# Kernel optimization log

Measured on AMD Instinct MI355X. Metric: run time of the kernel, lower is better.

Reference implementation:

```python
import jax, jax.numpy as jnp
import numpy as np

N = 100000
E = 1600000
K = 3
D_IN = 128
D_OUT = 128


def setup_inputs() -> dict:
    key = jax.random.key(0)
    ks = jax.random.split(key, 12)
    x = jax.random.normal(ks[0], (N, D_IN), dtype=jnp.float32)
    edge_index = jax.random.randint(ks[1], (2, E), 0, N, dtype=jnp.int64)
    hop_src = jax.random.randint(ks[2], (K, E), 0, N, dtype=jnp.int64)
    hop_dst = jax.random.randint(ks[3], (K, E), 0, N, dtype=jnp.int64)
    hop_vals = jax.random.uniform(ks[4], (K, E), dtype=jnp.float32) / 16.0  # ~normalized adj
    s = 1.0 / np.sqrt(D_IN)
    W_short = jax.random.normal(ks[5], (D_IN, D_OUT), dtype=jnp.float32) * s
    att_short_w = jax.random.normal(ks[6], (2 * D_OUT, 1), dtype=jnp.float32) * 0.05
    att_short_b = jnp.zeros((1,), dtype=jnp.float32)
    W_long = jax.random.normal(ks[7], (D_IN, D_OUT), dtype=jnp.float32) * s
    att_long_w = jax.random.normal(ks[8], (D_OUT, 1), dtype=jnp.float32) * 0.05
    att_long_b = jnp.zeros((1,), dtype=jnp.float32)
    return {"x": x, "edge_index": edge_index, "hop_src": hop_src, "hop_dst": hop_dst,
            "hop_vals": hop_vals, "W_short": W_short, "att_short_w": att_short_w,
            "att_short_b": att_short_b, "W_long": W_long, "att_long_w": att_long_w,
            "att_long_b": att_long_b}


def _leaky(x, slope):
    return jnp.where(x >= 0, x, slope * x)


def reference(x, edge_index, hop_src, hop_dst, hop_vals, W_short, att_short_w,
              att_short_b, W_long, att_long_w, att_long_b):
    # ---- ShortDistanceAttention (GAT-style gather-compute-scatter) ----
    h = x @ W_short                                   # [N, D]
    # att([x_i, x_j]) = x_i @ w[:D] + x_j @ w[D:] + b  (precompute per-node scalars)
    a_i = (h @ att_short_w[:D_OUT]).squeeze(-1)       # [N]
    a_j = (h @ att_short_w[D_OUT:]).squeeze(-1)       # [N]
    src, dst = edge_index[0], edge_index[1]
    score = jnp.exp(_leaky(a_i[dst] + a_j[src] + att_short_b[0], 0.2))  # [E]
    short = jax.ops.segment_sum(score[:, None] * h[src], dst, num_segments=N)  # [N, D]

    # ---- LongDistanceAttention (per-hop spmm + hop-softmax fusion) ----
    def hop_emb(s_idx, d_idx, vals):
        agg = jax.ops.segment_sum(vals[:, None] * x[s_idx], d_idx, num_segments=N)  # A_k @ x
        return _leaky(agg @ W_long, 0.01)             # [N, D]

    hk = jax.vmap(hop_emb)(hop_src, hop_dst, hop_vals)   # [K, N, D]
    hk = jnp.transpose(hk, (1, 0, 2))                    # [N, K, D]
    logits = hk @ att_long_w + att_long_b                # [N, K, 1]
    attn = jax.nn.softmax(logits, axis=1)                # softmax over hops
    long = jnp.sum(attn * hk, axis=1)                    # [N, D]

    return short + long
```

## Files before the change

### kernel.cpp

```cpp
#include <hip/hip_runtime.h>
#include <hip/hip_bf16.h>

#define NN 100000
#define EE 1600000
#define KK 3
#define DD 128
#define CAP 48

static __device__ __forceinline__ unsigned short f2bf(float f) {
  __hip_bfloat16 b = __float2bfloat16(f);
  return *reinterpret_cast<unsigned short*>(&b);
}

__global__ __launch_bounds__(256) void gemm_hy_kernel(
    const float* __restrict__ x, const float* __restrict__ Ws,
    const float* __restrict__ Wl, unsigned short* __restrict__ hb,
    unsigned short* __restrict__ yb, int N) {
  __shared__ float xs[64][36];
  __shared__ float ws[32][128];
  __shared__ float wl[32][128];

  const int n0 = blockIdx.x * 64;
  const int t = threadIdx.x;
  const int tc = t & 31;
  const int tr = t >> 5;
  const int col = tc * 4;
  const int row = tr * 8;

  float acch[8][4], accy[8][4];
#pragma unroll
  for (int i = 0; i < 8; ++i)
#pragma unroll
    for (int j = 0; j < 4; ++j) { acch[i][j] = 0.f; accy[i][j] = 0.f; }

  for (int kc = 0; kc < DD; kc += 32) {
    {
      int r = t >> 3;
      int c4 = (t & 7) * 4;
      int gn0 = n0 + r;
      int gn1 = n0 + r + 32;
      float4 v0 = make_float4(0, 0, 0, 0), v1 = make_float4(0, 0, 0, 0);
      if (gn0 < N) v0 = *(const float4*)&x[(size_t)gn0 * DD + kc + c4];
      if (gn1 < N) v1 = *(const float4*)&x[(size_t)gn1 * DD + kc + c4];
      *(float4*)&xs[r][c4] = v0;
      *(float4*)&xs[r + 32][c4] = v1;
    }
    {
      int c4w = (t & 31) * 4;
      int kr0 = t >> 5;
#pragma unroll
      for (int i = 0; i < 4; ++i) {
        int kr = kr0 + i * 8;
        *(float4*)&ws[kr][c4w] = *(const float4*)&Ws[(size_t)(kc + kr) * DD + c4w];
        *(float4*)&wl[kr][c4w] = *(const float4*)&Wl[(size_t)(kc + kr) * DD + c4w];
      }
    }
    __syncthreads();
#pragma unroll 4
    for (int kk = 0; kk < 32; ++kk) {
      float a[8];
#pragma unroll
      for (int i = 0; i < 8; ++i) a[i] = xs[row + i][kk];
      float4 b = *(const float4*)&ws[kk][col];
      float4 c = *(const float4*)&wl[kk][col];
#pragma unroll
      for (int i = 0; i < 8; ++i) {
        acch[i][0] += a[i] * b.x; acch[i][1] += a[i] * b.y;
        acch[i][2] += a[i] * b.z; acch[i][3] += a[i] * b.w;
        accy[i][0] += a[i] * c.x; accy[i][1] += a[i] * c.y;
        accy[i][2] += a[i] * c.z; accy[i][3] += a[i] * c.w;
      }
    }
    __syncthreads();
  }
#pragma unroll
  for (int i = 0; i < 8; ++i) {
    int gn = n0 + row + i;
    if (gn < N) {
      ushort4 oh, oy;
      oh.x = f2bf(acch[i][0]); oh.y = f2bf(acch[i][1]);
      oh.z = f2bf(acch[i][2]); oh.w = f2bf(acch[i][3]);
      oy.x = f2bf(accy[i][0]); oy.y = f2bf(accy[i][1]);
      oy.z = f2bf(accy[i][2]); oy.w = f2bf(accy[i][3]);
      *(ushort4*)&hb[(size_t)gn * DD + col] = oh;
      *(ushort4*)&yb[(size_t)gn * DD + col] = oy;
    }
  }
}

__global__ __launch_bounds__(256) void a_kernel(
    const unsigned short* __restrict__ hb, const float* __restrict__ asw,
    float* __restrict__ a_i, float* __restrict__ a_j, int N) {
  int n = (blockIdx.x * 256 + threadIdx.x) >> 6;
  if (n >= N) return;
  int lane = threadIdx.x & 63;
  unsigned int u = ((const unsigned int*)hb)[(size_t)n * (DD / 2) + lane];
  float v0 = __uint_as_float(u << 16);
  float v1 = __uint_as_float(u & 0xffff0000u);
  float2 wi = *(const float2*)&asw[lane * 2];
  float2 wj = *(const float2*)&asw[DD + lane * 2];
  float si = v0 * wi.x + v1 * wi.y;
  float sj = v0 * wj.x + v1 * wj.y;
#pragma unroll
  for (int m = 32; m > 0; m >>= 1) {
    si += __shfl_down(si, m);
    sj += __shfl_down(sj, m);
  }
  if (lane == 0) {
    a_i[n] = si;
    a_j[n] = sj;
  }
}

__global__ __launch_bounds__(256) void fill_short_kernel(
    const int* __restrict__ ei, const float* __restrict__ a_i,
    const float* __restrict__ a_j, const float* __restrict__ bias,
    int* __restrict__ cnt, int2* __restrict__ pair, int E) {
  float b = bias[0];
  for (int e = blockIdx.x * 256 + threadIdx.x; e < E; e += gridDim.x * 256) {
    int src = ei[e];
    int dst = ei[E + e];
    float z = a_i[dst] + a_j[src] + b;
    float sc = expf(z >= 0.f ? z : 0.2f * z);
    int pos = atomicAdd(&cnt[dst], 1);
    if (pos < CAP) pair[(size_t)dst * CAP + pos] = make_int2(src, __float_as_int(sc));
  }
}

__global__ __launch_bounds__(256) void fill_hop_kernel(
    const int* __restrict__ hsrc, const int* __restrict__ hdst,
    const float* __restrict__ hvals, int* __restrict__ cnt,
    int2* __restrict__ pair, int E) {
  for (int e = blockIdx.x * 256 + threadIdx.x; e < E; e += gridDim.x * 256) {
    int src = hsrc[e];
    int dst = hdst[e];
    float v = hvals[e];
    int pos = atomicAdd(&cnt[dst], 1);
    if (pos < CAP) pair[(size_t)dst * CAP + pos] = make_int2(src, __float_as_int(v));
  }
}

__global__ __launch_bounds__(256) void fused_pull_kernel(
    const int* __restrict__ cnt, const int2* __restrict__ pairs,
    const unsigned short* __restrict__ hb, const unsigned short* __restrict__ yb,
    const float* __restrict__ alw, const float* __restrict__ alb,
    float* __restrict__ out, int N) {
  int n = (blockIdx.x * 256 + threadIdx.x) >> 6;
  if (n >= N) return;
  int lane = threadIdx.x & 63;
  const unsigned int* hp = (const unsigned int*)hb;
  const unsigned int* yp = (const unsigned int*)yb;

  float sx = 0.f, sy = 0.f;
  {
    const int2* pb = pairs + (size_t)n * CAP;
    int d = min(cnt[n], CAP);
    int j = 0;
    for (; j + 1 < d; j += 2) {
      int2 p0 = pb[j], p1 = pb[j + 1];
      unsigned int u0 = hp[(size_t)p0.x * (DD / 2) + lane];
      unsigned int u1 = hp[(size_t)p1.x * (DD / 2) + lane];
      float w0 = __int_as_float(p0.y), w1 = __int_as_float(p1.y);
      sx += w0 * __uint_as_float(u0 << 16);
      sy += w0 * __uint_as_float(u0 & 0xffff0000u);
      sx += w1 * __uint_as_float(u1 << 16);
      sy += w1 * __uint_as_float(u1 & 0xffff0000u);
    }
    if (j < d) {
      int2 p = pb[j];
      unsigned int u = hp[(size_t)p.x * (DD / 2) + lane];
      float w = __int_as_float(p.y);
      sx += w * __uint_as_float(u << 16);
      sy += w * __uint_as_float(u & 0xffff0000u);
    }
  }

  float gx[3], gy[3];
#pragma unroll
  for (int k = 0; k < 3; ++k) {
    const int2* pb = pairs + ((size_t)(k + 1) * NN + n) * CAP;
    int d = min(cnt[(k + 1) * NN + n], CAP);
    float ax = 0.f, ay = 0.f;
    int j = 0;
    for (; j + 1 < d; j += 2) {
      int2 p0 = pb[j], p1 = pb[j + 1];
      unsigned int u0 = yp[(size_t)p0.x * (DD / 2) + lane];
      unsigned int u1 = yp[(size_t)p1.x * (DD / 2) + lane];
      float w0 = __int_as_float(p0.y), w1 = __int_as_float(p1.y);
      ax += w0 * __uint_as_float(u0 << 16);
      ay += w0 * __uint_as_float(u0 & 0xffff0000u);
      ax += w1 * __uint_as_float(u1 << 16);
      ay += w1 * __uint_as_float(u1 & 0xffff0000u);
    }
    if (j < d) {
      int2 p = pb[j];
      unsigned int u = yp[(size_t)p.x * (DD / 2) + lane];
      float w = __int_as_float(p.y);
      ax += w * __uint_as_float(u << 16);
      ay += w * __uint_as_float(u & 0xffff0000u);
    }
    gx[k] = ax >= 0.f ? ax : 0.01f * ax;
    gy[k] = ay >= 0.f ? ay : 0.01f * ay;
  }

  float2 aw = *(const float2*)&alw[lane * 2];
  float bl = alb[0];
  float lg[3];
#pragma unroll
  for (int k = 0; k < 3; ++k) {
    float p = gx[k] * aw.x + gy[k] * aw.y;
#pragma unroll
    for (int m = 1; m < 64; m <<= 1) p += __shfl_xor(p, m);
    lg[k] = p + bl;
  }
  float mx = fmaxf(lg[0], fmaxf(lg[1], lg[2]));
  float e0 = expf(lg[0] - mx), e1 = expf(lg[1] - mx), e2 = expf(lg[2] - mx);
  float inv = 1.f / (e0 + e1 + e2);
  e0 *= inv; e1 *= inv; e2 *= inv;

  float ox = sx + e0 * gx[0] + e1 * gx[1] + e2 * gx[2];
  float oy = sy + e0 * gy[0] + e1 * gy[1] + e2 * gy[2];
  *(float2*)&out[(size_t)n * DD + lane * 2] = make_float2(ox, oy);
}

extern "C" void kernel_launch(void* const* d_in, const int* in_sizes, int n_in,
                              void* d_out, int out_size, void* d_ws, size_t ws_size,
                              hipStream_t stream) {
  const float* x        = (const float*)d_in[0];
  const int*   ei       = (const int*)d_in[1];
  const int*   hsrc     = (const int*)d_in[2];
  const int*   hdst     = (const int*)d_in[3];
  const float* hvals    = (const float*)d_in[4];
  const float* W_short  = (const float*)d_in[5];
  const float* asw      = (const float*)d_in[6];
  const float* asb      = (const float*)d_in[7];
  const float* W_long   = (const float*)d_in[8];
  const float* alw      = (const float*)d_in[9];
  const float* alb      = (const float*)d_in[10];
  float* out = (float*)d_out;

  unsigned short* hb = (unsigned short*)d_ws;
  unsigned short* yb = hb + (size_t)NN * DD;
  float* a_i = (float*)(yb + (size_t)NN * DD);
  float* a_j = a_i + NN;
  int*   cnt = (int*)(a_j + NN);
  int2*  pair = (int2*)(cnt + 4 * NN);

  const int FG = 4096;
  const int PG = (NN * 64 + 255) / 256;
  const int GG = (NN + 63) / 64;

  gemm_hy_kernel<<<GG, 256, 0, stream>>>(x, W_short, W_long, hb, yb, NN);
  a_kernel<<<PG, 256, 0, stream>>>(hb, asw, a_i, a_j, NN);

  hipMemsetAsync(cnt, 0, 4 * NN * sizeof(int), stream);
  fill_short_kernel<<<FG, 256, 0, stream>>>(ei, a_i, a_j, asb, cnt, pair, EE);
  for (int k = 0; k < KK; ++k)
    fill_hop_kernel<<<FG, 256, 0, stream>>>(hsrc + (size_t)k * EE,
                                            hdst + (size_t)k * EE,
                                            hvals + (size_t)k * EE,
                                            cnt + (size_t)(k + 1) * NN,
                                            pair + (size_t)(k + 1) * NN * CAP, EE);

  fused_pull_kernel<<<PG, 256, 0, stream>>>(cnt, pair, hb, yb, alw, alb, out, NN);
}
```

Baseline: 982.6 us.

## Merge fill kernels and interleave four neighbor lists in pull kernel

Replaces the four per-list fill launches with a single kernel over all edge lists. Restructures the pull kernel so each wave stages its four neighbor lists in LDS, splits into half-waves that process alternating edges with 8-byte bf16 loads, and interleaves the short and three hop gathers in one loop. The goal is to raise memory-level parallelism in the gather-bound pull and cut launch overhead. In exchange it adds LDS traffic, divergent branches and a cross-half reduction, and lowers the fill grid size.

```diff
diff --git a/kernel.cpp b/kernel.cpp
--- a/kernel.cpp
+++ b/kernel.cpp
@@ -10,6 +10,12 @@
 static __device__ __forceinline__ unsigned short f2bf(float f) {
   __hip_bfloat16 b = __float2bfloat16(f);
   return *reinterpret_cast<unsigned short*>(&b);
+}
+static __device__ __forceinline__ float bflo(unsigned int v) {
+  return __uint_as_float(v << 16);
+}
+static __device__ __forceinline__ float bfhi(unsigned int v) {
+  return __uint_as_float(v & 0xffff0000u);
 }
 
 __global__ __launch_bounds__(256) void gemm_hy_kernel(
@@ -95,8 +101,8 @@
   if (n >= N) return;
   int lane = threadIdx.x & 63;
   unsigned int u = ((const unsigned int*)hb)[(size_t)n * (DD / 2) + lane];
-  float v0 = __uint_as_float(u << 16);
-  float v1 = __uint_as_float(u & 0xffff0000u);
+  float v0 = bflo(u);
+  float v1 = bfhi(u);
   float2 wi = *(const float2*)&asw[lane * 2];
   float2 wj = *(const float2*)&asw[DD + lane * 2];
   float si = v0 * wi.x + v1 * wi.y;
@@ -112,31 +118,35 @@
   }
 }
 
-__global__ __launch_bounds__(256) void fill_short_kernel(
-    const int* __restrict__ ei, const float* __restrict__ a_i,
-    const float* __restrict__ a_j, const float* __restrict__ bias,
-    int* __restrict__ cnt, int2* __restrict__ pair, int E) {
+__global__ __launch_bounds__(256) void fill_all_kernel(
+    const int* __restrict__ ei, const int* __restrict__ hsrc,
+    const int* __restrict__ hdst, const float* __restrict__ hvals,
+    const float* __restrict__ a_i, const float* __restrict__ a_j,
+    const float* __restrict__ bias, int* __restrict__ cnt,
+    int2* __restrict__ pair) {
   float b = bias[0];
-  for (int e = blockIdx.x * 256 + threadIdx.x; e < E; e += gridDim.x * 256) {
-    int src = ei[e];
-    int dst = ei[E + e];
-    float z = a_i[dst] + a_j[src] + b;
-    float sc = expf(z >= 0.f ? z : 0.2f * z);
-    int pos = atomicAdd(&cnt[dst], 1);
-    if (pos < CAP) pair[(size_t)dst * CAP + pos] = make_int2(src, __float_as_int(sc));
-  }
-}
-
-__global__ __launch_bounds__(256) void fill_hop_kernel(
-    const int* __restrict__ hsrc, const int* __restrict__ hdst,
-    const float* __restrict__ hvals, int* __restrict__ cnt,
-    int2* __restrict__ pair, int E) {
-  for (int e = blockIdx.x * 256 + threadIdx.x; e < E; e += gridDim.x * 256) {
-    int src = hsrc[e];
-    int dst = hdst[e];
-    float v = hvals[e];
-    int pos = atomicAdd(&cnt[dst], 1);
-    if (pos < CAP) pair[(size_t)dst * CAP + pos] = make_int2(src, __float_as_int(v));
+  const long TOT = 4L * EE;
+  for (long s = (long)blockIdx.x * 256 + threadIdx.x; s < TOT;
+       s += (long)gridDim.x * 256) {
+    int list = (int)(s / EE);
+    int e = (int)(s - (long)list * EE);
+    int src, dst;
+    float wv;
+    if (list == 0) {
+      src = ei[e];
+      dst = ei[EE + e];
+      float z = a_i[dst] + a_j[src] + b;
+      wv = expf(z >= 0.f ? z : 0.2f * z);
+    } else {
+      int k = list - 1;
+      src = hsrc[(size_t)k * EE + e];
+      dst = hdst[(size_t)k * EE + e];
+      wv = hvals[(size_t)k * EE + e];
+    }
+    int pos = atomicAdd(&cnt[(size_t)list * NN + dst], 1);
+    if (pos < CAP)
+      pair[((size_t)list * NN + dst) * CAP + pos] =
+          make_int2(src, __float_as_int(wv));
   }
 }
 
@@ -145,82 +155,111 @@
     const unsigned short* __restrict__ hb, const unsigned short* __restrict__ yb,
     const float* __restrict__ alw, const float* __restrict__ alb,
     float* __restrict__ out, int N) {
+  __shared__ int2 plds[4][4][CAP];
   int n = (blockIdx.x * 256 + threadIdx.x) >> 6;
   if (n >= N) return;
-  int lane = threadIdx.x & 63;
-  const unsigned int* hp = (const unsigned int*)hb;
-  const unsigned int* yp = (const unsigned int*)yb;
-
-  float sx = 0.f, sy = 0.f;
-  {
-    const int2* pb = pairs + (size_t)n * CAP;
-    int d = min(cnt[n], CAP);
-    int j = 0;
-    for (; j + 1 < d; j += 2) {
-      int2 p0 = pb[j], p1 = pb[j + 1];
-      unsigned int u0 = hp[(size_t)p0.x * (DD / 2) + lane];
-      unsigned int u1 = hp[(size_t)p1.x * (DD / 2) + lane];
-      float w0 = __int_as_float(p0.y), w1 = __int_as_float(p1.y);
-      sx += w0 * __uint_as_float(u0 << 16);
-      sy += w0 * __uint_as_float(u0 & 0xffff0000u);
-      sx += w1 * __uint_as_float(u1 << 16);
-      sy += w1 * __uint_as_float(u1 & 0xffff0000u);
-    }
-    if (j < d) {
-      int2 p = pb[j];
-      unsigned int u = hp[(size_t)p.x * (DD / 2) + lane];
-      float w = __int_as_float(p.y);
-      sx += w * __uint_as_float(u << 16);
-      sy += w * __uint_as_float(u & 0xffff0000u);
-    }
-  }
-
-  float gx[3], gy[3];
-#pragma unroll
-  for (int k = 0; k < 3; ++k) {
-    const int2* pb = pairs + ((size_t)(k + 1) * NN + n) * CAP;
-    int d = min(cnt[(k + 1) * NN + n], CAP);
-    float ax = 0.f, ay = 0.f;
-    int j = 0;
-    for (; j + 1 < d; j += 2) {
-      int2 p0 = pb[j], p1 = pb[j + 1];
-      unsigned int u0 = yp[(size_t)p0.x * (DD / 2) + lane];
-      unsigned int u1 = yp[(size_t)p1.x * (DD / 2) + lane];
-      float w0 = __int_as_float(p0.y), w1 = __int_as_float(p1.y);
-      ax += w0 * __uint_as_float(u0 << 16);
-      ay += w0 * __uint_as_float(u0 & 0xffff0000u);
-      ax += w1 * __uint_as_float(u1 << 16);
-      ay += w1 * __uint_as_float(u1 & 0xffff0000u);
-    }
-    if (j < d) {
-      int2 p = pb[j];
-      unsigned int u = yp[(size_t)p.x * (DD / 2) + lane];
-      float w = __int_as_float(p.y);
-      ax += w * __uint_as_float(u << 16);
-      ay += w * __uint_as_float(u & 0xffff0000u);
-    }
-    gx[k] = ax >= 0.f ? ax : 0.01f * ax;
-    gy[k] = ay >= 0.f ? ay : 0.01f * ay;
-  }
-
-  float2 aw = *(const float2*)&alw[lane * 2];
+  const int wv = threadIdx.x >> 6;
+  const int lane = threadIdx.x & 63;
+  const int half = lane >> 5;
+  const int l32 = lane & 31;
+
+  const uint2* hp = (const uint2*)hb;
+  const uint2* yp = (const uint2*)yb;
+
+  const int d0 = min(cnt[n], CAP);
+  const int d1 = min(cnt[NN + n], CAP);
+  const int d2 = min(cnt[2 * NN + n], CAP);
+  const int d3 = min(cnt[3 * NN + n], CAP);
+
+  if (lane < d0) plds[wv][0][lane] = pairs[(size_t)n * CAP + lane];
+  if (lane < d1) plds[wv][1][lane] = pairs[((size_t)NN + n) * CAP + lane];
+  if (lane < d2) plds[wv][2][lane] = pairs[((size_t)2 * NN + n) * CAP + lane];
+  if (lane < d3) plds[wv][3][lane] = pairs[((size_t)3 * NN + n) * CAP + lane];
+
+  float s0[4] = {0, 0, 0, 0};
+  float g0[4] = {0, 0, 0, 0}, g1[4] = {0, 0, 0, 0}, g2[4] = {0, 0, 0, 0};
+
+  int maxd = max(max(d0, d1), max(d2, d3));
+  for (int j = half; j < maxd; j += 2) {
+    uint2 u0, u1, u2, u3;
+    float w0 = 0.f, w1 = 0.f, w2 = 0.f, w3 = 0.f;
+    if (j < d0) {
+      int2 p = plds[wv][0][j];
+      w0 = __int_as_float(p.y);
+      u0 = hp[(size_t)p.x * 32 + l32];
+    }
+    if (j < d1) {
+      int2 p = plds[wv][1][j];
+      w1 = __int_as_float(p.y);
+      u1 = yp[(size_t)p.x * 32 + l32];
+    }
+    if (j < d2) {
+      int2 p = plds[wv][2][j];
+      w2 = __int_as_float(p.y);
+      u2 = yp[(size_t)p.x * 32 + l32];
+    }
+    if (j < d3) {
+      int2 p = plds[wv][3][j];
+      w3 = __int_as_float(p.y);
+      u3 = yp[(size_t)p.x * 32 + l32];
+    }
+    if (j < d0) {
+      s0[0] += w0 * bflo(u0.x); s0[1] += w0 * bfhi(u0.x);
+      s0[2] += w0 * bflo(u0.y); s0[3] += w0 * bfhi(u0.y);
+    }
+    if (j < d1) {
+      g0[0] += w1 * bflo(u1.x); g0[1] += w1 * bfhi(u1.x);
+      g0[2] += w1 * bflo(u1.y); g0[3] += w1 * bfhi(u1.y);
+    }
+    if (j < d2) {
+      g1[0] += w2 * bflo(u2.x); g1[1] += w2 * bfhi(u2.x);
+      g1[2] += w2 * bflo(u2.y); g1[3] += w2 * bfhi(u2.y);
+    }
+    if (j < d3) {
+      g2[0] += w3 * bflo(u3.x); g2[1] += w3 * bfhi(u3.x);
+      g2[2] += w3 * bflo(u3.y); g2[3] += w3 * bfhi(u3.y);
+    }
+  }
+
+#pragma unroll
+  for (int c = 0; c < 4; ++c) {
+    s0[c] += __shfl_xor(s0[c], 32);
+    g0[c] += __shfl_xor(g0[c], 32);
+    g1[c] += __shfl_xor(g1[c], 32);
+    g2[c] += __shfl_xor(g2[c], 32);
+    g0[c] = g0[c] >= 0.f ? g0[c] : 0.01f * g0[c];
+    g1[c] = g1[c] >= 0.f ? g1[c] : 0.01f * g1[c];
+    g2[c] = g2[c] >= 0.f ? g2[c] : 0.01f * g2[c];
+  }
+
+  float4 aw = *(const float4*)&alw[l32 * 4];
   float bl = alb[0];
   float lg[3];
-#pragma unroll
-  for (int k = 0; k < 3; ++k) {
-    float p = gx[k] * aw.x + gy[k] * aw.y;
-#pragma unroll
-    for (int m = 1; m < 64; m <<= 1) p += __shfl_xor(p, m);
-    lg[k] = p + bl;
+  {
+    float p0 = g0[0] * aw.x + g0[1] * aw.y + g0[2] * aw.z + g0[3] * aw.w;
+    float p1 = g1[0] * aw.x + g1[1] * aw.y + g1[2] * aw.z + g1[3] * aw.w;
+    float p2 = g2[0] * aw.x + g2[1] * aw.y + g2[2] * aw.z + g2[3] * aw.w;
+#pragma unroll
+    for (int m = 1; m < 32; m <<= 1) {
+      p0 += __shfl_xor(p0, m);
+      p1 += __shfl_xor(p1, m);
+      p2 += __shfl_xor(p2, m);
+    }
+    lg[0] = p0 + bl; lg[1] = p1 + bl; lg[2] = p2 + bl;
   }
   float mx = fmaxf(lg[0], fmaxf(lg[1], lg[2]));
   float e0 = expf(lg[0] - mx), e1 = expf(lg[1] - mx), e2 = expf(lg[2] - mx);
   float inv = 1.f / (e0 + e1 + e2);
   e0 *= inv; e1 *= inv; e2 *= inv;
 
-  float ox = sx + e0 * gx[0] + e1 * gx[1] + e2 * gx[2];
-  float oy = sy + e0 * gy[0] + e1 * gy[1] + e2 * gy[2];
-  *(float2*)&out[(size_t)n * DD + lane * 2] = make_float2(ox, oy);
+  if (half == 0) {
+    float4 o;
+    o.x = s0[0] + e0 * g0[0] + e1 * g1[0] + e2 * g2[0];
+    o.y = s0[1] + e0 * g0[1] + e1 * g1[1] + e2 * g2[1];
+    o.z = s0[2] + e0 * g0[2] + e1 * g1[2] + e2 * g2[2];
+    o.w = s0[3] + e0 * g0[3] + e1 * g1[3] + e2 * g2[3];
+    *(float4*)&out[(size_t)n * DD + l32 * 4] = o;
+  }
 }
 
 extern "C" void kernel_launch(void* const* d_in, const int* in_sizes, int n_in,
@@ -246,7 +285,7 @@
   int*   cnt = (int*)(a_j + NN);
   int2*  pair = (int2*)(cnt + 4 * NN);
 
-  const int FG = 4096;
+  const int FG = 2048;
   const int PG = (NN * 64 + 255) / 256;
   const int GG = (NN + 63) / 64;
 
@@ -254,13 +293,8 @@
   a_kernel<<<PG, 256, 0, stream>>>(hb, asw, a_i, a_j, NN);
 
   hipMemsetAsync(cnt, 0, 4 * NN * sizeof(int), stream);
-  fill_short_kernel<<<FG, 256, 0, stream>>>(ei, a_i, a_j, asb, cnt, pair, EE);
-  for (int k = 0; k < KK; ++k)
-    fill_hop_kernel<<<FG, 256, 0, stream>>>(hsrc + (size_t)k * EE,
-                                            hdst + (size_t)k * EE,
-                                            hvals + (size_t)k * EE,
-                                            cnt + (size_t)(k + 1) * NN,
-                                            pair + (size_t)(k + 1) * NN * CAP, EE);
+  fill_all_kernel<<<FG, 256, 0, stream>>>(ei, hsrc, hdst, hvals, a_i, a_j, asb,
+                                          cnt, pair);
 
   fused_pull_kernel<<<PG, 256, 0, stream>>>(cnt, pair, hb, yb, alw, alb, out, NN);
 }
```

After: 821.1 us. 16.4% less time.
